# Kernel optimization log

Hardware: AMD Instinct MI355X
Metric: run time of the kernel (lower is better)

## Reference

```python
import jax, jax.numpy as jnp
import numpy as np

S, I = 512, 384
C_MSA, C_Z, H, C = 64, 128, 8, 32
EPS = 1e-5


def _layernorm(x, g, b):
    mu = jnp.mean(x, axis=-1, keepdims=True)
    var = jnp.var(x, axis=-1, keepdims=True)
    return (x - mu) * jax.lax.rsqrt(var + EPS) * g + b


def setup_inputs() -> dict:
    key = jax.random.key(0)
    ks = jax.random.split(key, 6)
    sc_v = 1.0 / np.sqrt(C_MSA)
    sc_z = 1.0 / np.sqrt(C_Z)
    sc_o = 1.0 / np.sqrt(H * C)
    return {
        "msa_SI": jax.random.normal(ks[0], (S, I, C_MSA), jnp.float32),
        "pair_II": jax.random.normal(ks[1], (I, I, C_Z), jnp.float32),
        "ln_msa_g": jnp.ones((C_MSA,), jnp.float32),
        "ln_msa_b": jnp.zeros((C_MSA,), jnp.float32),
        "ln_pair_g": jnp.ones((C_Z,), jnp.float32),
        "ln_pair_b": jnp.zeros((C_Z,), jnp.float32),
        "W_v": jax.random.normal(ks[2], (C_MSA, H * C), jnp.float32) * sc_v,
        "W_bias": jax.random.normal(ks[3], (C_Z, H), jnp.float32) * sc_z,
        "W_gate": jax.random.normal(ks[4], (C_MSA, H * C), jnp.float32) * sc_v,
        "W_out": jax.random.normal(ks[5], (H * C, C_MSA), jnp.float32) * sc_o,
    }


def reference(msa_SI, pair_II, ln_msa_g, ln_msa_b, ln_pair_g, ln_pair_b,
              W_v, W_bias, W_gate, W_out):
    s, i = msa_SI.shape[:2]
    msa_n = _layernorm(msa_SI, ln_msa_g, ln_msa_b)              # [S,I,Cm]
    v_SIHC = (msa_n @ W_v).reshape(s, i, H, C)                   # [S,I,H,C]
    bias_IIH = _layernorm(pair_II, ln_pair_g, ln_pair_b) @ W_bias  # [I,I,H]
    w_IIH = jax.nn.softmax(bias_IIH, axis=-2)                    # softmax over j
    gate = jax.nn.sigmoid(msa_n @ W_gate)                        # [S,I,H*C]
    # weighted average shared across S: [I,I,H] x [S,I,H,C] -> [S,I,H,C]
    weights = jnp.einsum('ijh,sjhc->sihc', w_IIH, v_SIHC).reshape(s, i, H * C)
    o = gate * weights
    return o @ W_out                                             # [S,I,Cm]
```

## Files before the change

### kernel.cpp

```cpp
#include <hip/hip_runtime.h>
#include <hip/hip_bf16.h>

#define S_DIM 512
#define I_DIM 384
#define CM 64
#define CZ 128
#define H_DIM 8
#define C_DIM 32
#define HC 256
#define II (I_DIM*I_DIM)

typedef short bf16x8 __attribute__((ext_vector_type(8)));
typedef float f32x4 __attribute__((ext_vector_type(4)));

__device__ __forceinline__ float s2f(short s) {
    unsigned int u = ((unsigned int)(unsigned short)s) << 16;
    float f; __builtin_memcpy(&f, &u, 4); return f;
}
__device__ __forceinline__ short f2bf(float f) {
    __hip_bfloat16 h = __float2bfloat16(f);
    short r; __builtin_memcpy(&r, &h, 2); return r;
}

__device__ __forceinline__ void glds16(const short* g, short* l) {
    __builtin_amdgcn_global_load_lds(
        (const __attribute__((address_space(1))) void*)g,
        (__attribute__((address_space(3))) void*)l, 16, 0, 0);
}

__global__ __launch_bounds__(256) void k_pair_ln_bias(
    const float* __restrict__ pair, const float* __restrict__ g,
    const float* __restrict__ b, const float* __restrict__ Wb,
    float* __restrict__ bias)
{
    __shared__ float xs[4][CZ];
    __shared__ float WbT[H_DIM*132];
    const int tid = threadIdx.x;
    const int wv = tid >> 6, lane = tid & 63;
    const int ij = blockIdx.x*4 + wv;

    {
        float4 q = *(const float4*)(Wb + tid*4);
        int m = tid*4;
        WbT[(m&7)*132 + (m>>3)]     = q.x;
        WbT[((m+1)&7)*132 + ((m+1)>>3)] = q.y;
        WbT[((m+2)&7)*132 + ((m+2)>>3)] = q.z;
        WbT[((m+3)&7)*132 + ((m+3)>>3)] = q.w;
    }

    float2 x2 = *(const float2*)(pair + (size_t)ij*CZ + lane*2);
    float s1 = x2.x + x2.y;
    float s2 = x2.x*x2.x + x2.y*x2.y;
#pragma unroll
    for (int off = 32; off > 0; off >>= 1) {
        s1 += __shfl_xor(s1, off, 64);
        s2 += __shfl_xor(s2, off, 64);
    }
    float mu = s1 * (1.f/CZ);
    float var = s2 * (1.f/CZ) - mu*mu;
    float rs = rsqrtf(var + 1e-5f);
    xs[wv][lane*2]   = (x2.x - mu)*rs*g[lane*2]   + b[lane*2];
    xs[wv][lane*2+1] = (x2.y - mu)*rs*g[lane*2+1] + b[lane*2+1];
    __syncthreads();

    const int h = lane >> 3, seg = lane & 7;
    float p = 0.f;
#pragma unroll
    for (int jj = 0; jj < 16; jj++) {
        int c = seg + jj*8;
        p += xs[wv][c] * WbT[h*132 + c];
    }
    p += __shfl_down(p, 4, 64);
    p += __shfl_down(p, 2, 64);
    p += __shfl_down(p, 1, 64);
    if (seg == 0) bias[(size_t)h*II + ij] = p;
}

__global__ __launch_bounds__(384) void k_softmax(
    const float* __restrict__ bias, short* __restrict__ w)
{
    int blk = blockIdx.x;
    int i = blk >> 3, h = blk & 7;
    int j = threadIdx.x;
    float x = bias[(size_t)h*II + i*I_DIM + j];
    float m = x;
#pragma unroll
    for (int off = 32; off > 0; off >>= 1) m = fmaxf(m, __shfl_xor(m, off, 64));
    __shared__ float red[6];
    int wv = j >> 6;
    if ((j & 63) == 0) red[wv] = m;
    __syncthreads();
    m = red[0];
#pragma unroll
    for (int k = 1; k < 6; k++) m = fmaxf(m, red[k]);
    float e = __expf(x - m);
    float s = e;
#pragma unroll
    for (int off = 32; off > 0; off >>= 1) s += __shfl_xor(s, off, 64);
    __syncthreads();
    if ((j & 63) == 0) red[wv] = s;
    __syncthreads();
    s = 0.f;
#pragma unroll
    for (int k = 0; k < 6; k++) s += red[k];
    w[(size_t)h*II + i*I_DIM + j] = f2bf(e / s);
}

__global__ __launch_bounds__(256) void k_prep_w(
    const float* __restrict__ Wv, const float* __restrict__ Wg,
    const float* __restrict__ Wo,
    short* __restrict__ Wt, short* __restrict__ Wot)
{
    int idx = blockIdx.x*256 + threadIdx.x;
    if (idx < 512*64) {
        int n = idx >> 6, k = idx & 63;
        Wt[idx] = f2bf((n < HC) ? Wv[k*HC + n] : Wg[k*HC + (n - HC)]);
    } else {
        int q = idx - 512*64;
        int n = q >> 8, k = q & 255;
        Wot[q] = f2bf(Wo[k*64 + n]);
    }
}

__global__ __launch_bounds__(256) void k4_ln_vgate(
    const float* __restrict__ msa_c,
    const float* __restrict__ gm, const float* __restrict__ bm,
    const short* __restrict__ Wt,
    short* __restrict__ v_t, short* __restrict__ gate)
{
    __shared__ alignas(16) short lds[37376];
    short* As = lds;
    short* Bs = lds + 4608;
    short* Tv = lds;
    short* Tg = lds + 18432;

    const int tid = threadIdx.x;
    const int wave = tid >> 6;
    const int lane = tid & 63;
    const int pm = blockIdx.y;
    const int lr = lane >> 2, lq = lane & 3;
    const int fr = lane & 15, fq = lane >> 4;

#pragma unroll
    for (int kt = 0; kt < 2; kt++)
#pragma unroll
        for (int c2 = 0; c2 < 8; c2++) {
            int ch = wave + c2*4;
            glds16(Wt + (ch*16 + lr)*64 + kt*32 + lq*8,
                   &Bs[kt*16384 + ch*512]);
        }

    {
        const int row = tid >> 2;
        const int seg = tid & 3;
        float xf[16], gf[16], bf[16];
        const float* rp = msa_c + (size_t)(pm*64 + row)*CM + seg*16;
#pragma unroll
        for (int q = 0; q < 4; q++) {
            float4 a = *(const float4*)(rp + q*4);
            xf[q*4] = a.x; xf[q*4+1] = a.y; xf[q*4+2] = a.z; xf[q*4+3] = a.w;
            float4 gg = *(const float4*)(gm + seg*16 + q*4);
            gf[q*4] = gg.x; gf[q*4+1] = gg.y; gf[q*4+2] = gg.z; gf[q*4+3] = gg.w;
            float4 bb = *(const float4*)(bm + seg*16 + q*4);
            bf[q*4] = bb.x; bf[q*4+1] = bb.y; bf[q*4+2] = bb.z; bf[q*4+3] = bb.w;
        }
        float s1 = 0.f, s2 = 0.f;
#pragma unroll
        for (int j = 0; j < 16; j++) { s1 += xf[j]; s2 += xf[j]*xf[j]; }
        s1 += __shfl_xor(s1, 1); s2 += __shfl_xor(s2, 1);
        s1 += __shfl_xor(s1, 2); s2 += __shfl_xor(s2, 2);
        float mu = s1 * (1.f/64.f);
        float var = s2 * (1.f/64.f) - mu*mu;
        float rs = rsqrtf(var + 1e-5f);
        bf16x8 o0, o1;
#pragma unroll
        for (int j = 0; j < 8; j++) {
            o0[j] = f2bf((xf[j]   - mu)*rs*gf[j]   + bf[j]);
            o1[j] = f2bf((xf[8+j] - mu)*rs*gf[8+j] + bf[8+j]);
        }
        *(bf16x8*)&As[row*72 + seg*16]     = o0;
        *(bf16x8*)&As[row*72 + seg*16 + 8] = o1;
    }

    f32x4 acc[4][8] = {};
    __syncthreads();

#pragma unroll
    for (int kt = 0; kt < 2; ++kt) {
        bf16x8 af[4], bfrag[8];
#pragma unroll
        for (int mi = 0; mi < 4; mi++)
            af[mi] = *(const bf16x8*)&As[(mi*16 + fr)*72 + kt*32 + fq*8];
#pragma unroll
        for (int ni = 0; ni < 8; ni++)
            bfrag[ni] = *(const bf16x8*)
                &Bs[kt*16384 + (wave*128 + ni*16 + fr)*32 + fq*8];
#pragma unroll
        for (int mi = 0; mi < 4; mi++)
#pragma unroll
            for (int ni = 0; ni < 8; ni++)
                acc[mi][ni] = __builtin_amdgcn_mfma_f32_16x16x32_bf16(
                    af[mi], bfrag[ni], acc[mi][ni], 0, 0, 0);
    }
    __syncthreads();

    const int s_local = pm / 6;
    const int j0 = (pm % 6) * 64;
    if (wave < 2) {
#pragma unroll
        for (int mi = 0; mi < 4; mi++)
#pragma unroll
        for (int ni = 0; ni < 8; ni++) {
            int cl = wave*128 + ni*16 + fr;
            short4 pk;
            pk.x = f2bf(acc[mi][ni][0]);
            pk.y = f2bf(acc[mi][ni][1]);
            pk.z = f2bf(acc[mi][ni][2]);
            pk.w = f2bf(acc[mi][ni][3]);
            *(short4*)&Tv[cl*72 + mi*16 + fq*4] = pk;
        }
    } else {
#pragma unroll
        for (int mi = 0; mi < 4; mi++)
#pragma unroll
        for (int ni = 0; ni < 8; ni++)
#pragma unroll
        for (int r = 0; r < 4; r++) {
            int row = mi*16 + fq*4 + r;
            int col = (wave - 2)*128 + ni*16 + fr;
            Tg[row*264 + col] = f2bf(1.f/(1.f + __expf(-acc[mi][ni][r])));
        }
    }
    __syncthreads();

#pragma unroll
    for (int p = 0; p < 8; p++) {
        int unit = p*256 + tid;
        int cl = unit >> 3, part = unit & 7;
        bf16x8 d = *(const bf16x8*)&Tv[cl*72 + part*8];
        int h = cl >> 5, cc = cl & 31;
        *(bf16x8*)&v_t[(((size_t)s_local*H_DIM + h)*C_DIM + cc)*I_DIM + j0 + part*8] = d;
    }
#pragma unroll
    for (int p = 0; p < 8; p++) {
        int unit = p*256 + tid;
        int row = unit >> 5, ch = unit & 31;
        bf16x8 d = *(const bf16x8*)&Tg[row*264 + ch*8];
        *(bf16x8*)&gate[(size_t)(pm*64 + row)*HC + ch*8] = d;
    }
}

__global__ __launch_bounds__(512, 2) void k56_einsum_proj(
    const short* __restrict__ w,
    const short* __restrict__ v_t,
    const short* __restrict__ gate,
    const short* __restrict__ Wot,
    float* __restrict__ out)
{
    __shared__ alignas(16) short Ws[2][192*32];
    __shared__ alignas(16) short Vs[2][4][1024];
    __shared__ alignas(16) short Ob[8][32*40];
    const int tid = threadIdx.x;
    const int wave = tid >> 6, lane = tid & 63;
    const int fr = lane & 15, fq = lane >> 4;

    int bb = blockIdx.x;
    int ih, sg;
    if ((gridDim.x & 15) == 0) {
        int nb16 = gridDim.x >> 4;
        sg = (bb & 7)*nb16 + ((bb >> 3) >> 1);
        ih = (bb >> 3) & 1;
    } else { ih = bb & 1; sg = bb >> 1; }

    const int ibase = ih * 192;
    const int ms = wave >> 1;
    const int kv = wave & 1;
    const int s  = sg*4 + ms;
    const int iw = kv * 96;

    const int vs_s = wave >> 1;
    const int vs_h = wave & 1;
    const short* vstage = v_t + ((size_t)(sg*4 + vs_s)*H_DIM)*(C_DIM*I_DIM);

    auto stage = [&](int h_, int kt_, int buf) {
        const short* base = w + (size_t)h_*II + (size_t)kt_*32;
        {
            int row = wave*16 + (lane >> 2);
            int q = (lane & 3) ^ ((row >> 1) & 3);
            glds16(base + (size_t)(ibase + row)*I_DIM + q*8, &Ws[buf][wave*512]);
        }
        if (wave < 4) {
            int row = (8 + wave)*16 + (lane >> 2);
            int q = (lane & 3) ^ ((row >> 1) & 3);
            glds16(base + (size_t)(ibase + row)*I_DIM + q*8, &Ws[buf][(8+wave)*512]);
        }
        {
            int c = vs_h*16 + (lane >> 2);
            int q = (lane & 3) ^ ((c >> 1) & 3);
            glds16(vstage + (size_t)h_*(C_DIM*I_DIM) + (size_t)c*I_DIM + kt_*32 + q*8,
                   &Vs[buf][vs_s][vs_h*512]);
        }
    };

    f32x4 acc_o[6][4] = {};

    stage(0, 0, 0);
    stage(0, 1, 1);

#pragma unroll 1
    for (int h = 0; h < H_DIM; h++) {
        f32x4 acc_e[2][6] = {};
        short4 gv[2][6];
        bf16x8 bw[4];
#pragma unroll
        for (int kt = 0; kt < 12; kt++) {
            const int cb = kt & 1;
            if (wave < 4) asm volatile("s_waitcnt vmcnt(3)" ::: "memory");
            else          asm volatile("s_waitcnt vmcnt(2)" ::: "memory");
            __builtin_amdgcn_s_barrier();
            __builtin_amdgcn_sched_barrier(0);

            bf16x8 av[2], bwv[6];
#pragma unroll
            for (int mi = 0; mi < 2; mi++) {
                int row = mi*16 + fr;
                av[mi] = *(const bf16x8*)
                    &Vs[cb][ms][row*32 + ((fq ^ ((row >> 1) & 3)) << 3)];
            }
#pragma unroll
            for (int ni = 0; ni < 6; ni++) {
                int row = iw + ni*16 + fr;
                bwv[ni] = *(const bf16x8*)
                    &Ws[cb][row*32 + ((fq ^ ((row >> 1) & 3)) << 3)];
            }
            asm volatile("s_waitcnt lgkmcnt(0)" ::: "memory");
            __builtin_amdgcn_sched_barrier(0);
            __builtin_amdgcn_s_barrier();
            __builtin_amdgcn_sched_barrier(0);

            if (kt == 10) {
#pragma unroll
                for (int ni = 0; ni < 4; ni++)
                    bw[ni] = *(const bf16x8*)&Wot[(ni*16 + fr)*HC + h*C_DIM + fq*8];
#pragma unroll
                for (int mi = 0; mi < 2; mi++)
#pragma unroll
                for (int ni = 0; ni < 6; ni++)
                    gv[mi][ni] = *(const short4*)&gate[
                        (size_t)(s*I_DIM + ibase + iw + ni*16 + fr)*HC
                        + h*C_DIM + mi*16 + fq*4];
                __builtin_amdgcn_sched_barrier(0);
            }
            if (kt < 10)      stage(h, kt + 2, cb);
            else if (h < 7)   stage(h + 1, kt - 10, cb);
            __builtin_amdgcn_sched_barrier(0);

            __builtin_amdgcn_s_setprio(1);
#pragma unroll
            for (int mi = 0; mi < 2; mi++)
#pragma unroll
                for (int ni = 0; ni < 6; ni++)
                    acc_e[mi][ni] = __builtin_amdgcn_mfma_f32_16x16x32_bf16(
                        av[mi], bwv[ni], acc_e[mi][ni], 0, 0, 0);
            __builtin_amdgcn_s_setprio(0);
        }

        short* myOb = Ob[wave];
#pragma unroll
        for (int p = 0; p < 3; p++) {
#pragma unroll
            for (int t = 0; t < 2; t++) {
                int ni = p*2 + t;
#pragma unroll
                for (int mi = 0; mi < 2; mi++) {
                    short4 g = gv[mi][ni];
                    short4 pk;
                    pk.x = f2bf(acc_e[mi][ni][0] * s2f(g.x));
                    pk.y = f2bf(acc_e[mi][ni][1] * s2f(g.y));
                    pk.z = f2bf(acc_e[mi][ni][2] * s2f(g.z));
                    pk.w = f2bf(acc_e[mi][ni][3] * s2f(g.w));
                    *(short4*)&myOb[(t*16 + fr)*40 + mi*16 + fq*4] = pk;
                }
            }
            bf16x8 ao[2];
#pragma unroll
            for (int t = 0; t < 2; t++)
                ao[t] = *(const bf16x8*)&myOb[(t*16 + fr)*40 + fq*8];
            __builtin_amdgcn_s_setprio(1);
#pragma unroll
            for (int t = 0; t < 2; t++)
#pragma unroll
                for (int ni = 0; ni < 4; ni++)
                    acc_o[p*2 + t][ni] = __builtin_amdgcn_mfma_f32_16x16x32_bf16(
                        ao[t], bw[ni], acc_o[p*2 + t][ni], 0, 0, 0);
            __builtin_amdgcn_s_setprio(0);
        }
    }

#pragma unroll
    for (int mi = 0; mi < 6; mi++)
#pragma unroll
    for (int ni = 0; ni < 4; ni++)
#pragma unroll
    for (int r = 0; r < 4; r++) {
        int i = ibase + iw + mi*16 + fq*4 + r;
        int n = ni*16 + fr;
        out[(size_t)(s*I_DIM + i)*CM + n] = acc_o[mi][ni][r];
    }
}

extern "C" void kernel_launch(void* const* d_in, const int* in_sizes, int n_in,
                              void* d_out, int out_size, void* d_ws, size_t ws_size,
                              hipStream_t stream)
{
    const float* msa  = (const float*)d_in[0];
    const float* pair = (const float*)d_in[1];
    const float* gm   = (const float*)d_in[2];
    const float* bm   = (const float*)d_in[3];
    const float* gp   = (const float*)d_in[4];
    const float* bp   = (const float*)d_in[5];
    const float* Wv   = (const float*)d_in[6];
    const float* Wb   = (const float*)d_in[7];
    const float* Wg   = (const float*)d_in[8];
    const float* Wo   = (const float*)d_in[9];

    char* ws = (char*)d_ws;
    short* w    = (short*)ws;
    short* Wt   = (short*)(ws + 2359296);
    short* Wot  = (short*)(ws + 2424832);
    char*  region = ws + 2457600;
    float* bias = (float*)region;

    size_t avail = (ws_size > 2457600u) ? (ws_size - 2457600u) : 0;
    int Sc = 8;
    const int scs[7] = {512, 256, 128, 64, 32, 16, 8};
    for (int i = 0; i < 7; i++) {
        size_t need = (size_t)scs[i] * 393216u;
        if (need < 4718592u) need = 4718592u;
        if (need <= avail) { Sc = scs[i]; break; }
    }
    const int NC = S_DIM / Sc;
    short* v_t  = (short*)region;
    short* gate = (short*)(region + (size_t)Sc*196608u);

    k_pair_ln_bias<<<dim3(II/4), dim3(256), 0, stream>>>(pair, gp, bp, Wb, bias);
    k_prep_w<<<dim3(192), dim3(256), 0, stream>>>(Wv, Wg, Wo, Wt, Wot);
    k_softmax<<<dim3(I_DIM*H_DIM), dim3(I_DIM), 0, stream>>>(bias, w);

    for (int c = 0; c < NC; c++) {
        size_t in_off = (size_t)c * Sc * I_DIM * CM;

        k4_ln_vgate<<<dim3(1, Sc*6, 1), dim3(256), 0, stream>>>(
            msa + in_off, gm, bm, Wt, v_t, gate);

        k56_einsum_proj<<<dim3(Sc/2), dim3(512), 0, stream>>>(
            w, v_t, gate, Wot, (float*)d_out + in_off);
    }
}
```

Baseline: 422.5 us.

## Split einsum kernel i-range into quarters to double grid size

The fused einsum/projection kernel now covers 96 i-rows per block instead of 192, and the launch uses twice as many blocks. Per-wave tiles shrink from 6 to 3 column tiles, which lowers register and LDS use and raises parallelism and occupancy. In exchange each V tile in LDS is reused over half as many i-rows, so V is loaded from global memory twice as often and MFMA work per barrier drops.

```diff
diff --git a/kernel.cpp b/kernel.cpp
--- a/kernel.cpp
+++ b/kernel.cpp
@@ -257,42 +257,37 @@
     const short* __restrict__ Wot,
     float* __restrict__ out)
 {
-    __shared__ alignas(16) short Ws[2][192*32];
+    __shared__ alignas(16) short Ws[2][96*32];
     __shared__ alignas(16) short Vs[2][4][1024];
-    __shared__ alignas(16) short Ob[8][32*40];
+    __shared__ alignas(16) short Ob[8][48*40];
     const int tid = threadIdx.x;
     const int wave = tid >> 6, lane = tid & 63;
     const int fr = lane & 15, fq = lane >> 4;
 
     int bb = blockIdx.x;
-    int ih, sg;
-    if ((gridDim.x & 15) == 0) {
-        int nb16 = gridDim.x >> 4;
-        sg = (bb & 7)*nb16 + ((bb >> 3) >> 1);
-        ih = (bb >> 3) & 1;
-    } else { ih = bb & 1; sg = bb >> 1; }
-
-    const int ibase = ih * 192;
+    int iq, sg;
+    if ((gridDim.x & 31) == 0) {
+        int per = gridDim.x >> 5;
+        sg = (bb & 7)*per + ((bb >> 3) >> 2);
+        iq = (bb >> 3) & 3;
+    } else { iq = bb & 3; sg = bb >> 2; }
+
+    const int ibase = iq * 96;
     const int ms = wave >> 1;
     const int kv = wave & 1;
     const int s  = sg*4 + ms;
-    const int iw = kv * 96;
+    const int iw = kv * 48;
 
     const int vs_s = wave >> 1;
     const int vs_h = wave & 1;
     const short* vstage = v_t + ((size_t)(sg*4 + vs_s)*H_DIM)*(C_DIM*I_DIM);
 
     auto stage = [&](int h_, int kt_, int buf) {
-        const short* base = w + (size_t)h_*II + (size_t)kt_*32;
-        {
+        if (wave < 6) {
+            const short* base = w + (size_t)h_*II + (size_t)kt_*32;
             int row = wave*16 + (lane >> 2);
             int q = (lane & 3) ^ ((row >> 1) & 3);
             glds16(base + (size_t)(ibase + row)*I_DIM + q*8, &Ws[buf][wave*512]);
-        }
-        if (wave < 4) {
-            int row = (8 + wave)*16 + (lane >> 2);
-            int q = (lane & 3) ^ ((row >> 1) & 3);
-            glds16(base + (size_t)(ibase + row)*I_DIM + q*8, &Ws[buf][(8+wave)*512]);
         }
         {
             int c = vs_h*16 + (lane >> 2);
@@ -302,25 +297,25 @@
         }
     };
 
-    f32x4 acc_o[6][4] = {};
+    f32x4 acc_o[3][4] = {};
 
     stage(0, 0, 0);
     stage(0, 1, 1);
 
 #pragma unroll 1
     for (int h = 0; h < H_DIM; h++) {
-        f32x4 acc_e[2][6] = {};
-        short4 gv[2][6];
+        f32x4 acc_e[2][3] = {};
+        short4 gv[2][3];
         bf16x8 bw[4];
 #pragma unroll
         for (int kt = 0; kt < 12; kt++) {
             const int cb = kt & 1;
-            if (wave < 4) asm volatile("s_waitcnt vmcnt(3)" ::: "memory");
-            else          asm volatile("s_waitcnt vmcnt(2)" ::: "memory");
+            if (wave < 6) asm volatile("s_waitcnt vmcnt(2)" ::: "memory");
+            else          asm volatile("s_waitcnt vmcnt(1)" ::: "memory");
             __builtin_amdgcn_s_barrier();
             __builtin_amdgcn_sched_barrier(0);
 
-            bf16x8 av[2], bwv[6];
+            bf16x8 av[2], bwv[3];
 #pragma unroll
             for (int mi = 0; mi < 2; mi++) {
                 int row = mi*16 + fr;
@@ -328,7 +323,7 @@
                     &Vs[cb][ms][row*32 + ((fq ^ ((row >> 1) & 3)) << 3)];
             }
 #pragma unroll
-            for (int ni = 0; ni < 6; ni++) {
+            for (int ni = 0; ni < 3; ni++) {
                 int row = iw + ni*16 + fr;
                 bwv[ni] = *(const bf16x8*)
                     &Ws[cb][row*32 + ((fq ^ ((row >> 1) & 3)) << 3)];
@@ -345,7 +340,7 @@
 #pragma unroll
                 for (int mi = 0; mi < 2; mi++)
 #pragma unroll
-                for (int ni = 0; ni < 6; ni++)
+                for (int ni = 0; ni < 3; ni++)
                     gv[mi][ni] = *(const short4*)&gate[
                         (size_t)(s*I_DIM + ibase + iw + ni*16 + fr)*HC
                         + h*C_DIM + mi*16 + fq*4];
@@ -359,7 +354,7 @@
 #pragma unroll
             for (int mi = 0; mi < 2; mi++)
 #pragma unroll
-                for (int ni = 0; ni < 6; ni++)
+                for (int ni = 0; ni < 3; ni++)
                     acc_e[mi][ni] = __builtin_amdgcn_mfma_f32_16x16x32_bf16(
                         av[mi], bwv[ni], acc_e[mi][ni], 0, 0, 0);
             __builtin_amdgcn_s_setprio(0);
@@ -367,38 +362,33 @@
 
         short* myOb = Ob[wave];
 #pragma unroll
-        for (int p = 0; p < 3; p++) {
-#pragma unroll
-            for (int t = 0; t < 2; t++) {
-                int ni = p*2 + t;
-#pragma unroll
-                for (int mi = 0; mi < 2; mi++) {
-                    short4 g = gv[mi][ni];
-                    short4 pk;
-                    pk.x = f2bf(acc_e[mi][ni][0] * s2f(g.x));
-                    pk.y = f2bf(acc_e[mi][ni][1] * s2f(g.y));
-                    pk.z = f2bf(acc_e[mi][ni][2] * s2f(g.z));
-                    pk.w = f2bf(acc_e[mi][ni][3] * s2f(g.w));
-                    *(short4*)&myOb[(t*16 + fr)*40 + mi*16 + fq*4] = pk;
-                }
-            }
-            bf16x8 ao[2];
-#pragma unroll
-            for (int t = 0; t < 2; t++)
-                ao[t] = *(const bf16x8*)&myOb[(t*16 + fr)*40 + fq*8];
-            __builtin_amdgcn_s_setprio(1);
-#pragma unroll
-            for (int t = 0; t < 2; t++)
-#pragma unroll
-                for (int ni = 0; ni < 4; ni++)
-                    acc_o[p*2 + t][ni] = __builtin_amdgcn_mfma_f32_16x16x32_bf16(
-                        ao[t], bw[ni], acc_o[p*2 + t][ni], 0, 0, 0);
-            __builtin_amdgcn_s_setprio(0);
-        }
-    }
-
-#pragma unroll
-    for (int mi = 0; mi < 6; mi++)
+        for (int ni = 0; ni < 3; ni++)
+#pragma unroll
+        for (int mi = 0; mi < 2; mi++) {
+            short4 g = gv[mi][ni];
+            short4 pk;
+            pk.x = f2bf(acc_e[mi][ni][0] * s2f(g.x));
+            pk.y = f2bf(acc_e[mi][ni][1] * s2f(g.y));
+            pk.z = f2bf(acc_e[mi][ni][2] * s2f(g.z));
+            pk.w = f2bf(acc_e[mi][ni][3] * s2f(g.w));
+            *(short4*)&myOb[(ni*16 + fr)*40 + mi*16 + fq*4] = pk;
+        }
+        bf16x8 ao[3];
+#pragma unroll
+        for (int t = 0; t < 3; t++)
+            ao[t] = *(const bf16x8*)&myOb[(t*16 + fr)*40 + fq*8];
+        __builtin_amdgcn_s_setprio(1);
+#pragma unroll
+        for (int t = 0; t < 3; t++)
+#pragma unroll
+            for (int ni = 0; ni < 4; ni++)
+                acc_o[t][ni] = __builtin_amdgcn_mfma_f32_16x16x32_bf16(
+                    ao[t], bw[ni], acc_o[t][ni], 0, 0, 0);
+        __builtin_amdgcn_s_setprio(0);
+    }
+
+#pragma unroll
+    for (int mi = 0; mi < 3; mi++)
 #pragma unroll
     for (int ni = 0; ni < 4; ni++)
 #pragma unroll
@@ -453,7 +443,7 @@
         k4_ln_vgate<<<dim3(1, Sc*6, 1), dim3(256), 0, stream>>>(
             msa + in_off, gm, bm, Wt, v_t, gate);
 
-        k56_einsum_proj<<<dim3(Sc/2), dim3(512), 0, stream>>>(
+        k56_einsum_proj<<<dim3(Sc), dim3(512), 0, stream>>>(
             w, v_t, gate, Wot, (float*)d_out + in_off);
     }
 }
```

Result: slower. 434.5 us (+2.8%).

## Make pair-bias and LN/v-gate kernels persistent with software-prefetched MSA rows

Applied to the files above, without the earlier changes.

Converts k_pair_ln_bias into a grid-stride persistent kernel (1024 blocks) so the W_bias transpose and gamma/beta loads happen once per block rather than per 4 rows. Makes k4_ln_vgate persistent over at most 256 blocks, loading the W_v/W_gate weight tile into LDS once and double-buffering the next MSA row block in registers during the current block's MFMA and epilogue. Separate LDS regions for the transpose staging allow this overlap, at the cost of larger LDS use (occupancy 1) and more register pressure.

```diff
diff --git a/kernel.cpp b/kernel.cpp
--- a/kernel.cpp
+++ b/kernel.cpp
@@ -31,13 +31,12 @@
 __global__ __launch_bounds__(256) void k_pair_ln_bias(
     const float* __restrict__ pair, const float* __restrict__ g,
     const float* __restrict__ b, const float* __restrict__ Wb,
-    float* __restrict__ bias)
+    float* __restrict__ bias, int ngrp)
 {
     __shared__ float xs[4][CZ];
     __shared__ float WbT[H_DIM*132];
     const int tid = threadIdx.x;
     const int wv = tid >> 6, lane = tid & 63;
-    const int ij = blockIdx.x*4 + wv;
 
     {
         float4 q = *(const float4*)(Wb + tid*4);
@@ -47,33 +46,37 @@
         WbT[((m+2)&7)*132 + ((m+2)>>3)] = q.z;
         WbT[((m+3)&7)*132 + ((m+3)>>3)] = q.w;
     }
-
-    float2 x2 = *(const float2*)(pair + (size_t)ij*CZ + lane*2);
-    float s1 = x2.x + x2.y;
-    float s2 = x2.x*x2.x + x2.y*x2.y;
-#pragma unroll
-    for (int off = 32; off > 0; off >>= 1) {
-        s1 += __shfl_xor(s1, off, 64);
-        s2 += __shfl_xor(s2, off, 64);
-    }
-    float mu = s1 * (1.f/CZ);
-    float var = s2 * (1.f/CZ) - mu*mu;
-    float rs = rsqrtf(var + 1e-5f);
-    xs[wv][lane*2]   = (x2.x - mu)*rs*g[lane*2]   + b[lane*2];
-    xs[wv][lane*2+1] = (x2.y - mu)*rs*g[lane*2+1] + b[lane*2+1];
+    const float g0 = g[lane*2], g1 = g[lane*2+1];
+    const float b0 = b[lane*2], b1 = b[lane*2+1];
+    const int h = lane >> 3, seg = lane & 7;
     __syncthreads();
 
-    const int h = lane >> 3, seg = lane & 7;
-    float p = 0.f;
-#pragma unroll
-    for (int jj = 0; jj < 16; jj++) {
-        int c = seg + jj*8;
-        p += xs[wv][c] * WbT[h*132 + c];
-    }
-    p += __shfl_down(p, 4, 64);
-    p += __shfl_down(p, 2, 64);
-    p += __shfl_down(p, 1, 64);
-    if (seg == 0) bias[(size_t)h*II + ij] = p;
+    for (int grp = blockIdx.x; grp < ngrp; grp += gridDim.x) {
+        const int ij = grp*4 + wv;
+        float2 x2 = *(const float2*)(pair + (size_t)ij*CZ + lane*2);
+        float s1 = x2.x + x2.y;
+        float s2 = x2.x*x2.x + x2.y*x2.y;
+#pragma unroll
+        for (int off = 32; off > 0; off >>= 1) {
+            s1 += __shfl_xor(s1, off, 64);
+            s2 += __shfl_xor(s2, off, 64);
+        }
+        float mu = s1 * (1.f/CZ);
+        float var = s2 * (1.f/CZ) - mu*mu;
+        float rs = rsqrtf(var + 1e-5f);
+        xs[wv][lane*2]   = (x2.x - mu)*rs*g0 + b0;
+        xs[wv][lane*2+1] = (x2.y - mu)*rs*g1 + b1;
+        float p = 0.f;
+#pragma unroll
+        for (int jj = 0; jj < 16; jj++) {
+            int c = seg + jj*8;
+            p += xs[wv][c] * WbT[h*132 + c];
+        }
+        p += __shfl_down(p, 4, 64);
+        p += __shfl_down(p, 2, 64);
+        p += __shfl_down(p, 1, 64);
+        if (seg == 0) bias[(size_t)h*II + ij] = p;
+    }
 }
 
 __global__ __launch_bounds__(384) void k_softmax(
@@ -122,24 +125,23 @@
     }
 }
 
-__global__ __launch_bounds__(256) void k4_ln_vgate(
+__global__ __launch_bounds__(256, 1) void k4_ln_vgate(
     const float* __restrict__ msa_c,
     const float* __restrict__ gm, const float* __restrict__ bm,
     const short* __restrict__ Wt,
-    short* __restrict__ v_t, short* __restrict__ gate)
-{
-    __shared__ alignas(16) short lds[37376];
+    short* __restrict__ v_t, short* __restrict__ gate, int npm)
+{
+    __shared__ alignas(16) short lds[72704];
     short* As = lds;
     short* Bs = lds + 4608;
-    short* Tv = lds;
-    short* Tg = lds + 18432;
+    short* Tv = lds + 37376;
+    short* Tg = lds + 55808;
 
     const int tid = threadIdx.x;
-    const int wave = tid >> 6;
-    const int lane = tid & 63;
-    const int pm = blockIdx.y;
+    const int wave = tid >> 6, lane = tid & 63;
     const int lr = lane >> 2, lq = lane & 3;
     const int fr = lane & 15, fq = lane >> 4;
+    const int row = tid >> 2, seg = tid & 3;
 
 #pragma unroll
     for (int kt = 0; kt < 2; kt++)
@@ -150,23 +152,29 @@
                    &Bs[kt*16384 + ch*512]);
         }
 
-    {
-        const int row = tid >> 2;
-        const int seg = tid & 3;
-        float xf[16], gf[16], bf[16];
+    float gf[16], bf[16];
+#pragma unroll
+    for (int q = 0; q < 4; q++) {
+        float4 gg = *(const float4*)(gm + seg*16 + q*4);
+        gf[q*4] = gg.x; gf[q*4+1] = gg.y; gf[q*4+2] = gg.z; gf[q*4+3] = gg.w;
+        float4 bb = *(const float4*)(bm + seg*16 + q*4);
+        bf[q*4] = bb.x; bf[q*4+1] = bb.y; bf[q*4+2] = bb.z; bf[q*4+3] = bb.w;
+    }
+
+    auto ldmsa = [&](float (&xf)[16], int pm) {
         const float* rp = msa_c + (size_t)(pm*64 + row)*CM + seg*16;
 #pragma unroll
         for (int q = 0; q < 4; q++) {
             float4 a = *(const float4*)(rp + q*4);
             xf[q*4] = a.x; xf[q*4+1] = a.y; xf[q*4+2] = a.z; xf[q*4+3] = a.w;
-            float4 gg = *(const float4*)(gm + seg*16 + q*4);
-            gf[q*4] = gg.x; gf[q*4+1] = gg.y; gf[q*4+2] = gg.z; gf[q*4+3] = gg.w;
-            float4 bb = *(const float4*)(bm + seg*16 + q*4);
-            bf[q*4] = bb.x; bf[q*4+1] = bb.y; bf[q*4+2] = bb.z; bf[q*4+3] = bb.w;
-        }
+        }
+    };
+
+    auto body = [&](float (&xfC)[16], float (&xfN)[16], int pm, int pmN,
+                    bool pf) {
         float s1 = 0.f, s2 = 0.f;
 #pragma unroll
-        for (int j = 0; j < 16; j++) { s1 += xf[j]; s2 += xf[j]*xf[j]; }
+        for (int j = 0; j < 16; j++) { s1 += xfC[j]; s2 += xfC[j]*xfC[j]; }
         s1 += __shfl_xor(s1, 1); s2 += __shfl_xor(s2, 1);
         s1 += __shfl_xor(s1, 2); s2 += __shfl_xor(s2, 2);
         float mu = s1 * (1.f/64.f);
@@ -175,78 +183,96 @@
         bf16x8 o0, o1;
 #pragma unroll
         for (int j = 0; j < 8; j++) {
-            o0[j] = f2bf((xf[j]   - mu)*rs*gf[j]   + bf[j]);
-            o1[j] = f2bf((xf[8+j] - mu)*rs*gf[8+j] + bf[8+j]);
+            o0[j] = f2bf((xfC[j]   - mu)*rs*gf[j]   + bf[j]);
+            o1[j] = f2bf((xfC[8+j] - mu)*rs*gf[8+j] + bf[8+j]);
         }
         *(bf16x8*)&As[row*72 + seg*16]     = o0;
         *(bf16x8*)&As[row*72 + seg*16 + 8] = o1;
-    }
-
-    f32x4 acc[4][8] = {};
-    __syncthreads();
-
-#pragma unroll
-    for (int kt = 0; kt < 2; ++kt) {
-        bf16x8 af[4], bfrag[8];
-#pragma unroll
-        for (int mi = 0; mi < 4; mi++)
-            af[mi] = *(const bf16x8*)&As[(mi*16 + fr)*72 + kt*32 + fq*8];
-#pragma unroll
-        for (int ni = 0; ni < 8; ni++)
-            bfrag[ni] = *(const bf16x8*)
-                &Bs[kt*16384 + (wave*128 + ni*16 + fr)*32 + fq*8];
-#pragma unroll
-        for (int mi = 0; mi < 4; mi++)
+
+        __syncthreads();
+
+        f32x4 acc[4][8] = {};
+#pragma unroll
+        for (int kt = 0; kt < 2; ++kt) {
+            bf16x8 af[4], bfrag[8];
+#pragma unroll
+            for (int mi = 0; mi < 4; mi++)
+                af[mi] = *(const bf16x8*)&As[(mi*16 + fr)*72 + kt*32 + fq*8];
 #pragma unroll
             for (int ni = 0; ni < 8; ni++)
-                acc[mi][ni] = __builtin_amdgcn_mfma_f32_16x16x32_bf16(
-                    af[mi], bfrag[ni], acc[mi][ni], 0, 0, 0);
-    }
-    __syncthreads();
-
-    const int s_local = pm / 6;
-    const int j0 = (pm % 6) * 64;
-    if (wave < 2) {
-#pragma unroll
-        for (int mi = 0; mi < 4; mi++)
-#pragma unroll
-        for (int ni = 0; ni < 8; ni++) {
-            int cl = wave*128 + ni*16 + fr;
-            short4 pk;
-            pk.x = f2bf(acc[mi][ni][0]);
-            pk.y = f2bf(acc[mi][ni][1]);
-            pk.z = f2bf(acc[mi][ni][2]);
-            pk.w = f2bf(acc[mi][ni][3]);
-            *(short4*)&Tv[cl*72 + mi*16 + fq*4] = pk;
-        }
-    } else {
-#pragma unroll
-        for (int mi = 0; mi < 4; mi++)
-#pragma unroll
-        for (int ni = 0; ni < 8; ni++)
-#pragma unroll
-        for (int r = 0; r < 4; r++) {
-            int row = mi*16 + fq*4 + r;
-            int col = (wave - 2)*128 + ni*16 + fr;
-            Tg[row*264 + col] = f2bf(1.f/(1.f + __expf(-acc[mi][ni][r])));
-        }
-    }
-    __syncthreads();
-
-#pragma unroll
-    for (int p = 0; p < 8; p++) {
-        int unit = p*256 + tid;
-        int cl = unit >> 3, part = unit & 7;
-        bf16x8 d = *(const bf16x8*)&Tv[cl*72 + part*8];
-        int h = cl >> 5, cc = cl & 31;
-        *(bf16x8*)&v_t[(((size_t)s_local*H_DIM + h)*C_DIM + cc)*I_DIM + j0 + part*8] = d;
-    }
-#pragma unroll
-    for (int p = 0; p < 8; p++) {
-        int unit = p*256 + tid;
-        int row = unit >> 5, ch = unit & 31;
-        bf16x8 d = *(const bf16x8*)&Tg[row*264 + ch*8];
-        *(bf16x8*)&gate[(size_t)(pm*64 + row)*HC + ch*8] = d;
+                bfrag[ni] = *(const bf16x8*)
+                    &Bs[kt*16384 + (wave*128 + ni*16 + fr)*32 + fq*8];
+#pragma unroll
+            for (int mi = 0; mi < 4; mi++)
+#pragma unroll
+                for (int ni = 0; ni < 8; ni++)
+                    acc[mi][ni] = __builtin_amdgcn_mfma_f32_16x16x32_bf16(
+                        af[mi], bfrag[ni], acc[mi][ni], 0, 0, 0);
+        }
+
+        if (pf) ldmsa(xfN, pmN);
+
+        const int s_local = pm / 6;
+        const int j0 = (pm % 6) * 64;
+        if (wave < 2) {
+#pragma unroll
+            for (int mi = 0; mi < 4; mi++)
+#pragma unroll
+            for (int ni = 0; ni < 8; ni++) {
+                int cl = wave*128 + ni*16 + fr;
+                short4 pk;
+                pk.x = f2bf(acc[mi][ni][0]);
+                pk.y = f2bf(acc[mi][ni][1]);
+                pk.z = f2bf(acc[mi][ni][2]);
+                pk.w = f2bf(acc[mi][ni][3]);
+                *(short4*)&Tv[cl*72 + mi*16 + fq*4] = pk;
+            }
+        } else {
+#pragma unroll
+            for (int mi = 0; mi < 4; mi++)
+#pragma unroll
+            for (int ni = 0; ni < 8; ni++)
+#pragma unroll
+            for (int r = 0; r < 4; r++) {
+                int rw = mi*16 + fq*4 + r;
+                int col = (wave - 2)*128 + ni*16 + fr;
+                Tg[rw*264 + col] = f2bf(1.f/(1.f + __expf(-acc[mi][ni][r])));
+            }
+        }
+        __syncthreads();
+
+#pragma unroll
+        for (int p = 0; p < 8; p++) {
+            int unit = p*256 + tid;
+            int cl = unit >> 3, part = unit & 7;
+            bf16x8 d = *(const bf16x8*)&Tv[cl*72 + part*8];
+            int h = cl >> 5, cc = cl & 31;
+            *(bf16x8*)&v_t[(((size_t)s_local*H_DIM + h)*C_DIM + cc)*I_DIM
+                           + j0 + part*8] = d;
+        }
+#pragma unroll
+        for (int p = 0; p < 8; p++) {
+            int unit = p*256 + tid;
+            int rw = unit >> 5, ch = unit & 31;
+            bf16x8 d = *(const bf16x8*)&Tg[rw*264 + ch*8];
+            *(bf16x8*)&gate[(size_t)(pm*64 + rw)*HC + ch*8] = d;
+        }
+    };
+
+    float xfA[16], xfB[16];
+    int pm = blockIdx.x;
+    bool more = pm < npm;
+    if (more) ldmsa(xfA, pm);
+    while (more) {
+        int pmN = pm + 256;
+        bool moreN = pmN < npm;
+        body(xfA, xfB, pm, pmN, moreN);
+        pm = pmN; more = moreN;
+        if (!more) break;
+        pmN = pm + 256;
+        moreN = pmN < npm;
+        body(xfB, xfA, pm, pmN, moreN);
+        pm = pmN; more = moreN;
     }
 }
 
@@ -443,15 +469,18 @@
     short* v_t  = (short*)region;
     short* gate = (short*)(region + (size_t)Sc*196608u);
 
-    k_pair_ln_bias<<<dim3(II/4), dim3(256), 0, stream>>>(pair, gp, bp, Wb, bias);
+    k_pair_ln_bias<<<dim3(1024), dim3(256), 0, stream>>>(
+        pair, gp, bp, Wb, bias, II/4);
     k_prep_w<<<dim3(192), dim3(256), 0, stream>>>(Wv, Wg, Wo, Wt, Wot);
     k_softmax<<<dim3(I_DIM*H_DIM), dim3(I_DIM), 0, stream>>>(bias, w);
 
     for (int c = 0; c < NC; c++) {
         size_t in_off = (size_t)c * Sc * I_DIM * CM;
-
-        k4_ln_vgate<<<dim3(1, Sc*6, 1), dim3(256), 0, stream>>>(
-            msa + in_off, gm, bm, Wt, v_t, gate);
+        int npm = Sc * 6;
+        int k4grid = (npm < 256) ? npm : 256;
+
+        k4_ln_vgate<<<dim3(k4grid), dim3(256), 0, stream>>>(
+            msa + in_off, gm, bm, Wt, v_t, gate, npm);
 
         k56_einsum_proj<<<dim3(Sc/2), dim3(512), 0, stream>>>(
             w, v_t, gate, Wot, (float*)d_out + in_off);
```

Result: faster. 369.4 us (-12.6%).
